# Kernel optimization log

Hardware: AMD Instinct MI355X
Metric: run time of the kernel (lower is better)

The kernel has to match this reference:

```python
import jax, jax.numpy as jnp
import numpy as np

SEQ_LEN = 2048   # configs.seq_len == h == KFSSM H
PRED_LEN = 720   # configs.pred_len == p
D_MODEL = 128    # configs.d_model == KFSSM N (complex state size N//2)
C_OUT = 64       # configs.c_out == channel dim of u
BATCH = 128


def setup_inputs() -> dict:
    key = jax.random.key(0)
    ks = jax.random.split(key, 12)
    H, n2, p = SEQ_LEN, D_MODEL // 2, PRED_LEN
    u = jax.random.normal(ks[0], (BATCH, SEQ_LEN, C_OUT), jnp.float32)
    x_mark_enc = jax.random.normal(ks[1], (BATCH, SEQ_LEN, 4), jnp.float32)
    x_dec = jax.random.normal(ks[2], (BATCH, PRED_LEN, C_OUT), jnp.float32)
    x_mark_dec = jax.random.normal(ks[3], (BATCH, PRED_LEN, 4), jnp.float32)
    # standard-normal noise; scaled by learned std inside reference (matches torch.normal(0, std))
    W_noise = jax.random.normal(ks[4], (BATCH, SEQ_LEN, C_OUT), jnp.float32)
    # Model params
    D = jax.random.normal(ks[5], (H,), jnp.float32)
    log_variance = jnp.log(1.0 + jax.random.uniform(ks[6], (1,), jnp.float32))
    # KFSSM params
    C_param = jax.random.normal(ks[7], (H, n2, 2), jnp.float32)  # view_as_real of complex C
    log_dt = (jax.random.uniform(ks[8], (H,), jnp.float32)
              * (np.log(0.1) - np.log(0.001)) + np.log(0.001))
    log_A_real = jnp.log(0.5 * jnp.ones((H, n2), jnp.float32))
    A_imag = np.pi * jnp.tile(jnp.arange(n2, dtype=jnp.float32)[None, :], (H, 1))
    # outporj: Linear(h -> 2p) then GLU(dim=2)
    proj_w = jax.random.normal(ks[9], (2 * p, H), jnp.float32) * 0.02
    proj_b = jnp.zeros((2 * p,), jnp.float32)
    return dict(u=u, x_mark_enc=x_mark_enc, x_dec=x_dec, x_mark_dec=x_mark_dec,
                W_noise=W_noise, D=D, log_variance=log_variance, C_param=C_param,
                log_dt=log_dt, log_A_real=log_A_real, A_imag=A_imag,
                proj_w=proj_w, proj_b=proj_b)


def _ssm_kernels(Nl, C_param, log_dt, log_A_real, A_imag):
    # KFSSM.forward(N=Nl): returns K, K2 of shape (H, Nl)
    dt = jnp.exp(log_dt)                              # (H,)
    C = C_param[..., 0] + 1j * C_param[..., 1]        # (H, n2)
    A = -jnp.exp(log_A_real) + 1j * A_imag            # (H, n2)
    ar = jnp.arange(Nl, dtype=log_dt.dtype)
    Bk = A[:, :1] * ar[None, :] * dt[:, None]         # (H, Nl) complex
    dtA = A * dt[:, None]                             # (H, n2)
    Kexp = jnp.exp(dtA[:, :, None] * ar[None, None, :])  # (H, n2, Nl)
    Cc = C * (jnp.exp(dtA) - 1.0) / A                 # (H, n2)
    K = 2.0 * jnp.einsum('hn,hnl->hl', Cc, Kexp).real # (H, Nl)
    K2 = 2.0 * (K * Bk).real                          # (H, Nl)
    return K, K2


def reference(u, x_mark_enc, x_dec, x_mark_dec, W_noise, D, log_variance,
              C_param, log_dt, log_A_real, A_imag, proj_w, proj_b):
    # instance normalization over time
    x_mean = jnp.mean(u, axis=1, keepdims=True)                  # (B,1,N)
    u0 = u - x_mean
    x_var = jnp.var(u0, axis=1, ddof=1, keepdims=True) + 1e-5    # unbiased, as torch.var
    un = u0 / jnp.sqrt(x_var)
    # Kalman process noise
    std = jnp.sqrt(jnp.exp(log_variance))                        # (1,)
    W = std * W_noise                                            # (B,L,N)
    l, Nch = un.shape[1], un.shape[2]
    nfft = 2 * l
    K, K2 = _ssm_kernels(Nch, C_param, log_dt, log_A_real, A_imag)  # (H=l, Nch)
    k_f = jnp.fft.rfft(K.T, n=nfft, axis=-1)                     # (Nch, l+1)
    k2_f = jnp.fft.rfft(K2.T, n=nfft, axis=-1)
    u_f = jnp.fft.rfft(jnp.transpose(un, (0, 2, 1)), n=nfft, axis=-1)   # (B,Nch,l+1)
    w_f = jnp.fft.rfft(jnp.transpose(W, (0, 2, 1)), n=nfft, axis=-1)
    y = (jnp.fft.irfft(u_f * k2_f, n=nfft, axis=-1)
         + jnp.fft.irfft(w_f * k_f, n=nfft, axis=-1))            # (B,Nch,2l)
    y = jnp.transpose(y, (0, 2, 1))[:, -l:, :] + un * D[:, None] # (B,l,Nch)
    # outporj: Linear(h->2p) over time axis, then GLU(dim=2); Dropout1d is identity at eval
    z = jnp.einsum('bnh,ph->bnp', jnp.transpose(y, (0, 2, 1)), proj_w) + proj_b  # (B,Nch,2p)
    a, b = jnp.split(z, 2, axis=2)
    y = jnp.transpose(a * jax.nn.sigmoid(b), (0, 2, 1))          # (B,p,Nch)
    y = y * jnp.sqrt(x_var) + x_mean
    return y[:, -PRED_LEN:, :]
```

## Files before the change

### kernel.cpp

```cpp
#include <hip/hip_runtime.h>
#include <math.h>

typedef unsigned short u16;
typedef unsigned int u32;
typedef __attribute__((ext_vector_type(8))) short short8;
typedef __attribute__((ext_vector_type(4))) float f32x4;

#define B_   128
#define L_   2048
#define C_   64
#define P_   720
#define P2_  1440
#define NPAD 1536
#define NFFT 4096
#define NROW (B_*C_)
#define TCHUNK 16

__device__ __forceinline__ u16 f2bf(float f) {
  union { float f; unsigned u; } x; x.f = f;
  unsigned r = x.u + 0x7fffu + ((x.u >> 16) & 1u);
  return (u16)(r >> 16);
}
__device__ __forceinline__ float bf2f_lo(u32 v) {
  union { unsigned u; float f; } x; x.u = v << 16; return x.f;
}
__device__ __forceinline__ float bf2f_hi(u32 v) {
  union { unsigned u; float f; } x; x.u = v & 0xffff0000u; return x.f;
}

__device__ __forceinline__ float2 cmul(float2 a, float2 b) {
  return make_float2(a.x * b.x - a.y * b.y, a.x * b.y + a.y * b.x);
}
__device__ __forceinline__ float2 cadd(float2 a, float2 b) { return make_float2(a.x + b.x, a.y + b.y); }
__device__ __forceinline__ float2 csub(float2 a, float2 b) { return make_float2(a.x - b.x, a.y - b.y); }

#define CSWAP(i, j) { float2 tt = a[i]; a[i] = a[j]; a[j] = tt; }

template<bool INV, bool HZ>
__device__ __forceinline__ void dft16(float2 a[16]) {
  const float S  = INV ? 1.f : -1.f;
  const float c1 = 0.9238795325112867f, s1 = 0.3826834323650898f, q2 = 0.7071067811865476f;
  const float2 W1 = make_float2( c1, S * s1), W2 = make_float2( q2, S * q2), W3 = make_float2( s1, S * c1);
  const float2 W5 = make_float2(-s1, S * c1), W6 = make_float2(-q2, S * q2), W7 = make_float2(-c1, S * s1);
  if (HZ) {
    a[8]  = a[0];
    a[9]  = cmul(a[1], W1);
    a[10] = cmul(a[2], W2);
    a[11] = cmul(a[3], W3);
    a[12] = make_float2(-S * a[4].y, S * a[4].x);
    a[13] = cmul(a[5], W5);
    a[14] = cmul(a[6], W6);
    a[15] = cmul(a[7], W7);
  } else {
    float2 t;
    t = csub(a[0], a[8]);  a[0] = cadd(a[0], a[8]);  a[8]  = t;
    t = csub(a[1], a[9]);  a[1] = cadd(a[1], a[9]);  a[9]  = cmul(t, W1);
    t = csub(a[2], a[10]); a[2] = cadd(a[2], a[10]); a[10] = cmul(t, W2);
    t = csub(a[3], a[11]); a[3] = cadd(a[3], a[11]); a[11] = cmul(t, W3);
    t = csub(a[4], a[12]); a[4] = cadd(a[4], a[12]); a[12] = make_float2(-S * t.y, S * t.x);
    t = csub(a[5], a[13]); a[5] = cadd(a[5], a[13]); a[13] = cmul(t, W5);
    t = csub(a[6], a[14]); a[6] = cadd(a[6], a[14]); a[14] = cmul(t, W6);
    t = csub(a[7], a[15]); a[7] = cadd(a[7], a[15]); a[15] = cmul(t, W7);
  }
#pragma unroll
  for (int h = 0; h < 16; h += 8) {
    float2 t;
    t = csub(a[h+0], a[h+4]); a[h+0] = cadd(a[h+0], a[h+4]); a[h+4] = t;
    t = csub(a[h+1], a[h+5]); a[h+1] = cadd(a[h+1], a[h+5]); a[h+5] = cmul(t, W2);
    t = csub(a[h+2], a[h+6]); a[h+2] = cadd(a[h+2], a[h+6]); a[h+6] = make_float2(-S * t.y, S * t.x);
    t = csub(a[h+3], a[h+7]); a[h+3] = cadd(a[h+3], a[h+7]); a[h+7] = cmul(t, W6);
  }
#pragma unroll
  for (int q = 0; q < 16; q += 4) {
    float2 t;
    t = csub(a[q+0], a[q+2]); a[q+0] = cadd(a[q+0], a[q+2]); a[q+2] = t;
    t = csub(a[q+1], a[q+3]); a[q+1] = cadd(a[q+1], a[q+3]); a[q+3] = make_float2(-S * t.y, S * t.x);
  }
#pragma unroll
  for (int p = 0; p < 16; p += 2) {
    float2 t = csub(a[p], a[p+1]); a[p] = cadd(a[p], a[p+1]); a[p+1] = t;
  }
  CSWAP(1, 8); CSWAP(2, 4); CSWAP(3, 12); CSWAP(5, 10); CSWAP(7, 14); CSWAP(11, 13);
}

__device__ __forceinline__ void twchain(float2 a[16], float2 w1) {
  float2 w2 = cmul(w1, w1);
  float2 w3 = cmul(w2, w1);
  float2 w4 = cmul(w2, w2);
  float2 w5 = cmul(w3, w2);
  float2 w6 = cmul(w3, w3);
  float2 w7 = cmul(w4, w3);
  float2 w8 = cmul(w4, w4);
  float2 w9 = cmul(w5, w4);
  float2 w10 = cmul(w5, w5);
  float2 w11 = cmul(w6, w5);
  float2 w12 = cmul(w6, w6);
  float2 w13 = cmul(w7, w6);
  float2 w14 = cmul(w7, w7);
  float2 w15 = cmul(w8, w7);
  a[1]  = cmul(a[1],  w1);  a[2]  = cmul(a[2],  w2);  a[3]  = cmul(a[3],  w3);
  a[4]  = cmul(a[4],  w4);  a[5]  = cmul(a[5],  w5);  a[6]  = cmul(a[6],  w6);
  a[7]  = cmul(a[7],  w7);  a[8]  = cmul(a[8],  w8);  a[9]  = cmul(a[9],  w9);
  a[10] = cmul(a[10], w10); a[11] = cmul(a[11], w11); a[12] = cmul(a[12], w12);
  a[13] = cmul(a[13], w13); a[14] = cmul(a[14], w14); a[15] = cmul(a[15], w15);
}

__device__ __forceinline__ void lds_wA(float2* X, const float2 r[16], int tid) {
  int base = (tid & 15) * 16 + ((tid >> 4) ^ ((tid & 7) << 1));
#pragma unroll
  for (int i = 0; i < 16; ++i) X[base + i * 256] = r[i];
}
__device__ __forceinline__ void lds_wB(float2* X, const float2 r[16], int tid) {
#pragma unroll
  for (int i = 0; i < 16; ++i)
    X[((tid & 0xF0) + i) * 16 + ((tid & 15) ^ ((i & 7) << 1))] = r[i];
}
__device__ __forceinline__ void lds_rd(const float2* X, float2 r[16], int tid) {
  const float4* X4 = (const float4*)X;
#pragma unroll
  for (int p = 0; p < 8; ++p) {
    float4 v = X4[tid * 8 + (p ^ (tid & 7))];
    r[2 * p]     = make_float2(v.x, v.y);
    r[2 * p + 1] = make_float2(v.z, v.w);
  }
}

__device__ __forceinline__ void fft_fwd_hz(float2 r[16], float2* X, int tid, const float2* twg) {
  dft16<false, true>(r);
  twchain(r, twg[tid]);
  lds_wA(X, r, tid);
  __syncthreads();
  lds_rd(X, r, tid);
  dft16<false, false>(r);
  twchain(r, twg[(tid & 15) << 4]);
  __syncthreads();
  lds_wB(X, r, tid);
  __syncthreads();
  lds_rd(X, r, tid);
  dft16<false, false>(r);
}

__device__ __forceinline__ void fft_inv(float2 r[16], float2* X, int tid, const float2* twg) {
  dft16<true, false>(r);
  __syncthreads();
  lds_wB(X, r, tid);
  __syncthreads();
  lds_rd(X, r, tid);
  float2 wb = twg[(tid & 15) << 4];
  twchain(r, make_float2(wb.x, -wb.y));
  dft16<true, false>(r);
  __syncthreads();
  lds_wA(X, r, tid);
  __syncthreads();
  lds_rd(X, r, tid);
  float2 wa = twg[tid];
  twchain(r, make_float2(wa.x, -wa.y));
  dft16<true, false>(r);
}

__global__ void k_twfill(float2* __restrict__ tw) {
  int k = threadIdx.x;
  double ang = -2.0 * 3.14159265358979323846 * (double)k / 4096.0;
  tw[k] = make_float2((float)cos(ang), (float)sin(ang));
}

__global__ void k_wconv(const float* __restrict__ pw, u16* __restrict__ wb) {
  size_t idx = (size_t)blockIdx.x * 256 + threadIdx.x;
  int n = (int)(idx >> 11);
  int k = (int)(idx & 2047);
  int q = n >> 1;
  float v = 0.f;
  if (q < P_) {
    int p = (n & 1) ? (P_ + q) : q;
    v = pw[(size_t)p * L_ + k];
  }
  wb[idx] = f2bf(v);
}

__global__ __launch_bounds__(256) void k_stats1(const float* __restrict__ u, float* __restrict__ ps,
                                                float* __restrict__ pq) {
  int blk = blockIdx.x;
  int b = blk >> 4, q = blk & 15;
  int tid = threadIdx.x;
  int c4 = tid & 15, g = tid >> 4;
  const float4* u4 = (const float4*)(u + ((size_t)b * L_ + q * 128) * C_);
  float4 s = make_float4(0.f, 0.f, 0.f, 0.f), sq = s;
#pragma unroll
  for (int i = 0; i < 8; ++i) {
    float4 v = u4[(size_t)(g + 16 * i) * 16 + c4];
    s.x += v.x; s.y += v.y; s.z += v.z; s.w += v.w;
    sq.x += v.x * v.x; sq.y += v.y * v.y; sq.z += v.z * v.z; sq.w += v.w * v.w;
  }
  __shared__ float4 sb[16][16], qb[16][16];
  sb[g][c4] = s; qb[g][c4] = sq;
  __syncthreads();
  if (g == 0) {
    float4 S = sb[0][c4], Q = qb[0][c4];
#pragma unroll
    for (int k = 1; k < 16; ++k) {
      float4 a = sb[k][c4], d = qb[k][c4];
      S.x += a.x; S.y += a.y; S.z += a.z; S.w += a.w;
      Q.x += d.x; Q.y += d.y; Q.z += d.z; Q.w += d.w;
    }
    ((float4*)ps)[blk * 16 + c4] = S;
    ((float4*)pq)[blk * 16 + c4] = Q;
  }
}

__global__ __launch_bounds__(256) void k_stats2(const float* __restrict__ ps, const float* __restrict__ pq,
                                                float4* __restrict__ mv) {
  int gid = blockIdx.x * 256 + threadIdx.x;
  int b = gid >> 6, c = gid & 63;
  float S = 0.f, Q = 0.f;
#pragma unroll
  for (int q = 0; q < 16; ++q) {
    S += ps[(size_t)(b * 16 + q) * 64 + c];
    Q += pq[(size_t)(b * 16 + q) * 64 + c];
  }
  float mean = S * (1.0f / 2048.0f);
  float var = (Q - S * S * (1.0f / 2048.0f)) * (1.0f / 2047.0f) + 1e-5f;
  float sv = sqrtf(var);
  mv[gid] = make_float4(mean, sv, 1.0f / sv, 0.0f);
}

__global__ __launch_bounds__(256) void k_ssmk(const float* __restrict__ Cp, const float* __restrict__ ldt,
                                              const float* __restrict__ lAr, const float* __restrict__ Aim,
                                              float2* __restrict__ kz) {
  int gid = blockIdx.x * 256 + threadIdx.x;
  int h = gid & 2047;
  int j = gid >> 11;
  float dt = expf(ldt[h]);
  float accx = 0.f;
  float Ar0 = 0.f;
  for (int n = 0; n < 64; ++n) {
    float Ar = -expf(lAr[h * 64 + n]);
    float Ai = Aim[h * 64 + n];
    if (n == 0) Ar0 = Ar;
    float dAr = Ar * dt, dAi = Ai * dt;
    float er = expf(dAr);
    float s1, c1; sincosf(dAi, &s1, &c1);
    float emr = er * c1 - 1.0f, emi = er * s1;
    float inv = 1.0f / (Ar * Ar + Ai * Ai);
    float qr = (emr * Ar + emi * Ai) * inv;
    float qi = (emi * Ar - emr * Ai) * inv;
    float cr = Cp[(size_t)(h * 64 + n) * 2];
    float ci = Cp[(size_t)(h * 64 + n) * 2 + 1];
    float ccr = cr * qr - ci * qi;
    float cci = cr * qi + ci * qr;
    float ej = expf(dAr * (float)j);
    float sj, cj; sincosf(dAi * (float)j, &sj, &cj);
    accx += ccr * (ej * cj) - cci * (ej * sj);
  }
  float K = 2.0f * accx;
  float K2 = 2.0f * K * (Ar0 * (float)j * dt);
  kz[(size_t)j * L_ + h] = make_float2(K2, -K);
}

__global__ __launch_bounds__(256) void k_packT(const float* __restrict__ u, const float* __restrict__ Wn,
                                               const float* __restrict__ lv, const float4* __restrict__ mv,
                                               u32* __restrict__ zu) {
  int b = blockIdx.x >> 5;
  int t0 = (blockIdx.x & 31) << 6;
  int tid = threadIdx.x;
  float stdn = sqrtf(__expf(lv[0]));
  __shared__ float2 tile[64][65];
  int c = tid & 63, r = tid >> 6;
  float4 m = mv[b * C_ + c];
#pragma unroll
  for (int i = 0; i < 16; ++i) {
    int t = t0 + i * 4 + r;
    size_t idx = ((size_t)b * L_ + t) * C_ + c;
    float uu = (u[idx] - m.x) * m.z;
    float ww = Wn[idx] * stdn;
    tile[i * 4 + r][c] = make_float2(uu, ww);
  }
  __syncthreads();
  int t = tid & 63, cb = tid >> 6;
#pragma unroll
  for (int i = 0; i < 16; ++i) {
    int c2 = i * 4 + cb;
    float2 v = tile[t][c2];
    zu[((size_t)(b * C_ + c2)) * L_ + t0 + t] = ((u32)f2bf(v.y) << 16) | (u32)f2bf(v.x);
  }
}

__global__ __launch_bounds__(256) void k_fftk(const float2* __restrict__ kz, const float2* __restrict__ twg,
                                              float2* __restrict__ G) {
  __shared__ float2 X[NFFT];
  int j = blockIdx.x, tid = threadIdx.x;
  float2 r[16];
#pragma unroll
  for (int n2 = 0; n2 < 8; ++n2) r[n2] = kz[(size_t)j * L_ + n2 * 256 + tid];
  fft_fwd_hz(r, X, tid, twg);
  const float sc = 1.0f / 4096.0f;
#pragma unroll
  for (int k0 = 0; k0 < 16; ++k0)
    G[(size_t)j * NFFT + k0 * 256 + tid] = make_float2(r[k0].x * sc, r[k0].y * sc);
}

__global__ __launch_bounds__(256) void k_fftmain(const u32* __restrict__ zu, const float2* __restrict__ twg,
                                                 const float2* __restrict__ G, const float* __restrict__ Dv,
                                                 u16* __restrict__ yT) {
  __shared__ float2 X[NFFT];
  int row = blockIdx.x;
  int j = row & 63;
  int tid = threadIdx.x;
  float2 r[16];
  float usav[8];
#pragma unroll
  for (int n2 = 0; n2 < 8; ++n2) {
    u32 v = zu[(size_t)row * L_ + n2 * 256 + tid];
    float uu = bf2f_lo(v), ww = bf2f_hi(v);
    r[n2] = make_float2(uu, ww);
    usav[n2] = uu;
  }
  fft_fwd_hz(r, X, tid, twg);
  const float2* Gj = G + (size_t)j * NFFT;
#pragma unroll
  for (int k0 = 0; k0 < 16; ++k0) r[k0] = cmul(r[k0], Gj[k0 * 256 + tid]);
  fft_inv(r, X, tid, twg);
#pragma unroll
  for (int n2 = 8; n2 < 16; ++n2) {
    int t = (n2 - 8) * 256 + tid;
    float yv = r[n2].x + usav[n2 - 8] * Dv[t];
    yT[(size_t)row * L_ + t] = f2bf(yv);
  }
}

__device__ __forceinline__ int lds_ix(int row, int slot) {
  return row * 32 + ((slot ^ ((row >> 1) & 3)) << 3);
}

__global__ __launch_bounds__(256) void k_gemm(const u16* __restrict__ A, const u16* __restrict__ B,
                                              const float* __restrict__ pb, const float4* __restrict__ mv,
                                              float* __restrict__ out) {
  __shared__ u16 As[128 * 32];
  __shared__ u16 Bs[128 * 32];
  __shared__ float ob[32 * 132];
  const int K = L_;
  int tid = threadIdx.x;
  int bid = blockIdx.x;
  int swz = (bid & 7) * 96 + (bid >> 3);
  int bm = swz % 64, bn = swz / 64;
  int wave = tid >> 6, lane = tid & 63;
  int wm = (wave >> 1) << 6, wn = (wave & 1) << 6;
  int lr = lane & 15, lk = lane >> 4;
  int trow = tid >> 2, tslot = tid & 3;
  const u16* Ag = A + (size_t)(bm * 128 + trow) * K + tslot * 8;
  const u16* Bg = B + (size_t)(bn * 128 + trow) * K + tslot * 8;
  f32x4 acc[4][4] = {};
  uint4 pa0 = *(const uint4*)(Ag);
  uint4 pa1 = *(const uint4*)(Ag + (size_t)64 * K);
  uint4 pb0 = *(const uint4*)(Bg);
  uint4 pb1 = *(const uint4*)(Bg + (size_t)64 * K);
  for (int kt = 0; kt < K; kt += 32) {
    __syncthreads();
    *(uint4*)&As[lds_ix(trow, tslot)] = pa0;
    *(uint4*)&As[lds_ix(trow + 64, tslot)] = pa1;
    *(uint4*)&Bs[lds_ix(trow, tslot)] = pb0;
    *(uint4*)&Bs[lds_ix(trow + 64, tslot)] = pb1;
    __syncthreads();
    if (kt + 32 < K) {
      pa0 = *(const uint4*)(Ag + kt + 32);
      pa1 = *(const uint4*)(Ag + (size_t)64 * K + kt + 32);
      pb0 = *(const uint4*)(Bg + kt + 32);
      pb1 = *(const uint4*)(Bg + (size_t)64 * K + kt + 32);
    }
    short8 af[4], bf[4];
#pragma unroll
    for (int i2 = 0; i2 < 4; ++i2) af[i2] = *(const short8*)&As[lds_ix(wm + i2 * 16 + lr, lk)];
#pragma unroll
    for (int j2 = 0; j2 < 4; ++j2) bf[j2] = *(const short8*)&Bs[lds_ix(wn + j2 * 16 + lr, lk)];
#pragma unroll
    for (int i2 = 0; i2 < 4; ++i2)
#pragma unroll
      for (int j2 = 0; j2 < 4; ++j2)
        acc[i2][j2] = __builtin_amdgcn_mfma_f32_16x16x32_bf16(af[i2], bf[j2], acc[i2][j2], 0, 0, 0);
  }
  int col_lo = wn + lr;
  for (int chunk = 0; chunk < 2; ++chunk) {
    __syncthreads();
#pragma unroll
    for (int j2c = 0; j2c < 2; ++j2c) {
      int j2 = chunk * 2 + j2c;
      int col = col_lo + j2 * 16;
      int nglob = bn * 128 + col;
      int q = nglob >> 1;
      float bias = 0.f;
      if (q < P_) bias = pb[(nglob & 1) ? (P_ + q) : q];
      int qloc = col >> 1;
      int s = (qloc & 15) | ((qloc >> 5) << 4);
#pragma unroll
      for (int i2 = 0; i2 < 4; ++i2) {
        int row = wm + i2 * 16 + lk * 4;
        float res[4];
#pragma unroll
        for (int rgi = 0; rgi < 4; ++rgi) {
          float val = acc[i2][j2][rgi] + bias;
          float other = __shfl_xor(val, 1);
          float4 m = mv[bm * 128 + row + rgi];
          res[rgi] = val * (1.0f / (1.0f + __expf(-other))) * m.y + m.x;
        }
        if (!(lane & 1)) {
          *(float4*)&ob[s * 132 + row] = make_float4(res[0], res[1], res[2], res[3]);
        }
      }
    }
    __syncthreads();
    int c = tid & 63, sl4 = tid >> 6;
    for (int rd = 0; rd < 16; ++rd) {
      int slice = rd * 4 + sl4;
      int s = slice >> 1, bb = slice & 1;
      int qloc = (s & 15) + chunk * 16 + ((s >> 4) << 5);
      int qglob = bn * 64 + qloc;
      if (qglob < P_) {
        int bg = bm * 2 + bb;
        out[((size_t)bg * P_ + qglob) * 64 + c] = ob[s * 132 + bb * 64 + c];
      }
    }
  }
}

extern "C" void kernel_launch(void* const* d_in, const int* in_sizes, int n_in,
                              void* d_out, int out_size, void* d_ws, size_t ws_size,
                              hipStream_t stream) {
  const float* u   = (const float*)d_in[0];
  const float* Wn  = (const float*)d_in[4];
  const float* Dv  = (const float*)d_in[5];
  const float* lv  = (const float*)d_in[6];
  const float* Cp  = (const float*)d_in[7];
  const float* ldt = (const float*)d_in[8];
  const float* lAr = (const float*)d_in[9];
  const float* Aim = (const float*)d_in[10];
  const float* pw  = (const float*)d_in[11];
  const float* pb  = (const float*)d_in[12];
  float* out = (float*)d_out;
  char* ws = (char*)d_ws;

  float2* tw = (float2*)(ws + 0);
  float4* mv = (float4*)(ws + (64 << 10));
  float2* G  = (float2*)(ws + (1 << 20));
  float2* kz = (float2*)(ws + (3 << 20));
  u16*    Wb = (u16*)   (ws + (4 << 20));
  float*  ps = (float*) (ws + (10 << 20));
  float*  pq = (float*) (ws + (10 << 20) + (512 << 10));
  u16*    yT = (u16*)   (ws + (16 << 20));
  u32*    zu = (u32*)   (ws + ((size_t)48 << 20));

  k_twfill<<<1, 256, 0, stream>>>(tw);
  k_wconv<<<(NPAD * L_) / 256, 256, 0, stream>>>(pw, Wb);
  k_stats1<<<B_ * TCHUNK, 256, 0, stream>>>(u, ps, pq);
  k_stats2<<<(B_ * C_) / 256, 256, 0, stream>>>(ps, pq, mv);
  k_ssmk<<<(C_ * L_) / 256, 256, 0, stream>>>(Cp, ldt, lAr, Aim, kz);
  k_packT<<<B_ * (L_ / 64), 256, 0, stream>>>(u, Wn, lv, mv, zu);
  k_fftk<<<C_, 256, 0, stream>>>(kz, tw, G);
  k_fftmain<<<NROW, 256, 0, stream>>>(zu, tw, G, Dv, yT);
  k_gemm<<<64 * (NPAD / 128), 256, 0, stream>>>(yT, Wb, pb, mv, out);
}
```

Measured before the change: 343.1 us.

## Merge independent prep kernels into two multi-role launches by block-index dispatch

Seven small setup kernels (twiddle fill, weight bf16 conversion, stats partials, stats finalize, SSM kernel generation, pack/transposition, kernel FFT) are combined into two launches. Blocks branch on blockIdx into roles, so independent work runs concurrently and launch gaps shrink. Each pack block recomputes the per-batch mean/var from the partial sums in LDS instead of waiting on a separate stats2 kernel. The full mv array is still written by extra blocks for the GEMM. The cost is redundant stats reduction work and a larger shared-memory footprint for every block in the merged kernel.

New measurement: 324.9 us. 5.3% less time.

```diff
diff --git a/kernel.cpp b/kernel.cpp
--- a/kernel.cpp
+++ b/kernel.cpp
@@ -15,6 +15,13 @@
 #define NFFT 4096
 #define NROW (B_*C_)
 #define TCHUNK 16
+
+#define PREP_SSMK   512
+#define PREP_STATS1 2048
+#define PREP_NB     (PREP_SSMK + PREP_STATS1 + 1 + (NPAD * L_) / 256)
+#define PF_PACK  4096
+#define PF_FFTK  64
+#define PF_NB    (PF_PACK + PF_FFTK + 32)
 
 __device__ __forceinline__ u16 f2bf(float f) {
   union { float f; unsigned u; } x; x.f = f;
@@ -158,144 +165,157 @@
   dft16<true, false>(r);
 }
 
-__global__ void k_twfill(float2* __restrict__ tw) {
-  int k = threadIdx.x;
-  double ang = -2.0 * 3.14159265358979323846 * (double)k / 4096.0;
-  tw[k] = make_float2((float)cos(ang), (float)sin(ang));
-}
-
-__global__ void k_wconv(const float* __restrict__ pw, u16* __restrict__ wb) {
-  size_t idx = (size_t)blockIdx.x * 256 + threadIdx.x;
-  int n = (int)(idx >> 11);
-  int k = (int)(idx & 2047);
-  int q = n >> 1;
-  float v = 0.f;
-  if (q < P_) {
-    int p = (n & 1) ? (P_ + q) : q;
-    v = pw[(size_t)p * L_ + k];
-  }
-  wb[idx] = f2bf(v);
-}
-
-__global__ __launch_bounds__(256) void k_stats1(const float* __restrict__ u, float* __restrict__ ps,
-                                                float* __restrict__ pq) {
-  int blk = blockIdx.x;
-  int b = blk >> 4, q = blk & 15;
-  int tid = threadIdx.x;
-  int c4 = tid & 15, g = tid >> 4;
-  const float4* u4 = (const float4*)(u + ((size_t)b * L_ + q * 128) * C_);
-  float4 s = make_float4(0.f, 0.f, 0.f, 0.f), sq = s;
-#pragma unroll
-  for (int i = 0; i < 8; ++i) {
-    float4 v = u4[(size_t)(g + 16 * i) * 16 + c4];
-    s.x += v.x; s.y += v.y; s.z += v.z; s.w += v.w;
-    sq.x += v.x * v.x; sq.y += v.y * v.y; sq.z += v.z * v.z; sq.w += v.w * v.w;
-  }
+__global__ __launch_bounds__(256) void k_prep(const float* __restrict__ pw, u16* __restrict__ wb,
+                                              const float* __restrict__ u, float* __restrict__ ps,
+                                              float* __restrict__ pq,
+                                              const float* __restrict__ Cp, const float* __restrict__ ldt,
+                                              const float* __restrict__ lAr, const float* __restrict__ Aim,
+                                              float2* __restrict__ kz, float2* __restrict__ tw) {
   __shared__ float4 sb[16][16], qb[16][16];
-  sb[g][c4] = s; qb[g][c4] = sq;
-  __syncthreads();
-  if (g == 0) {
-    float4 S = sb[0][c4], Q = qb[0][c4];
-#pragma unroll
-    for (int k = 1; k < 16; ++k) {
-      float4 a = sb[k][c4], d = qb[k][c4];
-      S.x += a.x; S.y += a.y; S.z += a.z; S.w += a.w;
-      Q.x += d.x; Q.y += d.y; Q.z += d.z; Q.w += d.w;
-    }
-    ((float4*)ps)[blk * 16 + c4] = S;
-    ((float4*)pq)[blk * 16 + c4] = Q;
-  }
-}
-
-__global__ __launch_bounds__(256) void k_stats2(const float* __restrict__ ps, const float* __restrict__ pq,
-                                                float4* __restrict__ mv) {
-  int gid = blockIdx.x * 256 + threadIdx.x;
-  int b = gid >> 6, c = gid & 63;
-  float S = 0.f, Q = 0.f;
-#pragma unroll
-  for (int q = 0; q < 16; ++q) {
-    S += ps[(size_t)(b * 16 + q) * 64 + c];
-    Q += pq[(size_t)(b * 16 + q) * 64 + c];
-  }
-  float mean = S * (1.0f / 2048.0f);
-  float var = (Q - S * S * (1.0f / 2048.0f)) * (1.0f / 2047.0f) + 1e-5f;
-  float sv = sqrtf(var);
-  mv[gid] = make_float4(mean, sv, 1.0f / sv, 0.0f);
-}
-
-__global__ __launch_bounds__(256) void k_ssmk(const float* __restrict__ Cp, const float* __restrict__ ldt,
-                                              const float* __restrict__ lAr, const float* __restrict__ Aim,
-                                              float2* __restrict__ kz) {
-  int gid = blockIdx.x * 256 + threadIdx.x;
-  int h = gid & 2047;
-  int j = gid >> 11;
-  float dt = expf(ldt[h]);
-  float accx = 0.f;
-  float Ar0 = 0.f;
-  for (int n = 0; n < 64; ++n) {
-    float Ar = -expf(lAr[h * 64 + n]);
-    float Ai = Aim[h * 64 + n];
-    if (n == 0) Ar0 = Ar;
-    float dAr = Ar * dt, dAi = Ai * dt;
-    float er = expf(dAr);
-    float s1, c1; sincosf(dAi, &s1, &c1);
-    float emr = er * c1 - 1.0f, emi = er * s1;
-    float inv = 1.0f / (Ar * Ar + Ai * Ai);
-    float qr = (emr * Ar + emi * Ai) * inv;
-    float qi = (emi * Ar - emr * Ai) * inv;
-    float cr = Cp[(size_t)(h * 64 + n) * 2];
-    float ci = Cp[(size_t)(h * 64 + n) * 2 + 1];
-    float ccr = cr * qr - ci * qi;
-    float cci = cr * qi + ci * qr;
-    float ej = expf(dAr * (float)j);
-    float sj, cj; sincosf(dAi * (float)j, &sj, &cj);
-    accx += ccr * (ej * cj) - cci * (ej * sj);
-  }
-  float K = 2.0f * accx;
-  float K2 = 2.0f * K * (Ar0 * (float)j * dt);
-  kz[(size_t)j * L_ + h] = make_float2(K2, -K);
-}
-
-__global__ __launch_bounds__(256) void k_packT(const float* __restrict__ u, const float* __restrict__ Wn,
-                                               const float* __restrict__ lv, const float4* __restrict__ mv,
-                                               u32* __restrict__ zu) {
-  int b = blockIdx.x >> 5;
-  int t0 = (blockIdx.x & 31) << 6;
-  int tid = threadIdx.x;
-  float stdn = sqrtf(__expf(lv[0]));
-  __shared__ float2 tile[64][65];
-  int c = tid & 63, r = tid >> 6;
-  float4 m = mv[b * C_ + c];
-#pragma unroll
-  for (int i = 0; i < 16; ++i) {
-    int t = t0 + i * 4 + r;
-    size_t idx = ((size_t)b * L_ + t) * C_ + c;
-    float uu = (u[idx] - m.x) * m.z;
-    float ww = Wn[idx] * stdn;
-    tile[i * 4 + r][c] = make_float2(uu, ww);
-  }
-  __syncthreads();
-  int t = tid & 63, cb = tid >> 6;
-#pragma unroll
-  for (int i = 0; i < 16; ++i) {
-    int c2 = i * 4 + cb;
-    float2 v = tile[t][c2];
-    zu[((size_t)(b * C_ + c2)) * L_ + t0 + t] = ((u32)f2bf(v.y) << 16) | (u32)f2bf(v.x);
-  }
-}
-
-__global__ __launch_bounds__(256) void k_fftk(const float2* __restrict__ kz, const float2* __restrict__ twg,
-                                              float2* __restrict__ G) {
-  __shared__ float2 X[NFFT];
-  int j = blockIdx.x, tid = threadIdx.x;
-  float2 r[16];
-#pragma unroll
-  for (int n2 = 0; n2 < 8; ++n2) r[n2] = kz[(size_t)j * L_ + n2 * 256 + tid];
-  fft_fwd_hz(r, X, tid, twg);
-  const float sc = 1.0f / 4096.0f;
-#pragma unroll
-  for (int k0 = 0; k0 < 16; ++k0)
-    G[(size_t)j * NFFT + k0 * 256 + tid] = make_float2(r[k0].x * sc, r[k0].y * sc);
+  int blk = blockIdx.x, tid = threadIdx.x;
+  if (blk < PREP_SSMK) {
+    int gid = blk * 256 + tid;
+    int h = gid & 2047;
+    int j = gid >> 11;
+    float dt = expf(ldt[h]);
+    float accx = 0.f;
+    float Ar0 = 0.f;
+    for (int n = 0; n < 64; ++n) {
+      float Ar = -expf(lAr[h * 64 + n]);
+      float Ai = Aim[h * 64 + n];
+      if (n == 0) Ar0 = Ar;
+      float dAr = Ar * dt, dAi = Ai * dt;
+      float er = expf(dAr);
+      float s1, c1; sincosf(dAi, &s1, &c1);
+      float emr = er * c1 - 1.0f, emi = er * s1;
+      float inv = 1.0f / (Ar * Ar + Ai * Ai);
+      float qr = (emr * Ar + emi * Ai) * inv;
+      float qi = (emi * Ar - emr * Ai) * inv;
+      float cr = Cp[(size_t)(h * 64 + n) * 2];
+      float ci = Cp[(size_t)(h * 64 + n) * 2 + 1];
+      float ccr = cr * qr - ci * qi;
+      float cci = cr * qi + ci * qr;
+      float ej = expf(dAr * (float)j);
+      float sj, cj; sincosf(dAi * (float)j, &sj, &cj);
+      accx += ccr * (ej * cj) - cci * (ej * sj);
+    }
+    float K = 2.0f * accx;
+    float K2 = 2.0f * K * (Ar0 * (float)j * dt);
+    kz[(size_t)j * L_ + h] = make_float2(K2, -K);
+  } else if (blk < PREP_SSMK + PREP_STATS1) {
+    int blk2 = blk - PREP_SSMK;
+    int b = blk2 >> 4, q = blk2 & 15;
+    int c4 = tid & 15, g = tid >> 4;
+    const float4* u4 = (const float4*)(u + ((size_t)b * L_ + q * 128) * C_);
+    float4 s = make_float4(0.f, 0.f, 0.f, 0.f), sq = s;
+#pragma unroll
+    for (int i = 0; i < 8; ++i) {
+      float4 v = u4[(size_t)(g + 16 * i) * 16 + c4];
+      s.x += v.x; s.y += v.y; s.z += v.z; s.w += v.w;
+      sq.x += v.x * v.x; sq.y += v.y * v.y; sq.z += v.z * v.z; sq.w += v.w * v.w;
+    }
+    sb[g][c4] = s; qb[g][c4] = sq;
+    __syncthreads();
+    if (g == 0) {
+      float4 S = sb[0][c4], Q = qb[0][c4];
+#pragma unroll
+      for (int k = 1; k < 16; ++k) {
+        float4 a = sb[k][c4], d = qb[k][c4];
+        S.x += a.x; S.y += a.y; S.z += a.z; S.w += a.w;
+        Q.x += d.x; Q.y += d.y; Q.z += d.z; Q.w += d.w;
+      }
+      ((float4*)ps)[blk2 * 16 + c4] = S;
+      ((float4*)pq)[blk2 * 16 + c4] = Q;
+    }
+  } else if (blk == PREP_SSMK + PREP_STATS1) {
+    int k = tid;
+    double ang = -2.0 * 3.14159265358979323846 * (double)k / 4096.0;
+    tw[k] = make_float2((float)cos(ang), (float)sin(ang));
+  } else {
+    size_t idx = (size_t)(blk - (PREP_SSMK + PREP_STATS1 + 1)) * 256 + tid;
+    int n = (int)(idx >> 11);
+    int k = (int)(idx & 2047);
+    int q = n >> 1;
+    float v = 0.f;
+    if (q < P_) {
+      int p = (n & 1) ? (P_ + q) : q;
+      v = pw[(size_t)p * L_ + k];
+    }
+    wb[idx] = f2bf(v);
+  }
+}
+
+__global__ __launch_bounds__(256) void k_packfftk(const float* __restrict__ u, const float* __restrict__ Wn,
+                                                  const float* __restrict__ lv,
+                                                  const float* __restrict__ ps, const float* __restrict__ pq,
+                                                  u32* __restrict__ zu,
+                                                  const float2* __restrict__ kz, const float2* __restrict__ twg,
+                                                  float2* __restrict__ G, float4* __restrict__ mv) {
+  __shared__ __align__(16) char smem[33280];
+  int blk = blockIdx.x, tid = threadIdx.x;
+  if (blk < PF_PACK) {
+    int b = blk >> 5;
+    int t0 = (blk & 31) << 6;
+    float4* mvs = (float4*)smem;
+    if (tid < 64) {
+      float S = 0.f, Q = 0.f;
+#pragma unroll
+      for (int q = 0; q < 16; ++q) {
+        S += ps[(size_t)(b * 16 + q) * 64 + tid];
+        Q += pq[(size_t)(b * 16 + q) * 64 + tid];
+      }
+      float mean = S * (1.0f / 2048.0f);
+      float var = (Q - S * S * (1.0f / 2048.0f)) * (1.0f / 2047.0f) + 1e-5f;
+      float sv = sqrtf(var);
+      mvs[tid] = make_float4(mean, sv, 1.0f / sv, 0.0f);
+    }
+    __syncthreads();
+    int c = tid & 63, r = tid >> 6;
+    float4 m = mvs[c];
+    float stdn = sqrtf(__expf(lv[0]));
+    __syncthreads();
+    float2 (*tile)[65] = (float2(*)[65])smem;
+#pragma unroll
+    for (int i = 0; i < 16; ++i) {
+      int t = t0 + i * 4 + r;
+      size_t idx = ((size_t)b * L_ + t) * C_ + c;
+      float uu = (u[idx] - m.x) * m.z;
+      float ww = Wn[idx] * stdn;
+      tile[i * 4 + r][c] = make_float2(uu, ww);
+    }
+    __syncthreads();
+    int t = tid & 63, cb = tid >> 6;
+#pragma unroll
+    for (int i = 0; i < 16; ++i) {
+      int c2 = i * 4 + cb;
+      float2 v = tile[t][c2];
+      zu[((size_t)(b * C_ + c2)) * L_ + t0 + t] = ((u32)f2bf(v.y) << 16) | (u32)f2bf(v.x);
+    }
+  } else if (blk < PF_PACK + PF_FFTK) {
+    float2* X = (float2*)smem;
+    int j = blk - PF_PACK;
+    float2 r[16];
+#pragma unroll
+    for (int n2 = 0; n2 < 8; ++n2) r[n2] = kz[(size_t)j * L_ + n2 * 256 + tid];
+    fft_fwd_hz(r, X, tid, twg);
+    const float sc = 1.0f / 4096.0f;
+#pragma unroll
+    for (int k0 = 0; k0 < 16; ++k0)
+      G[(size_t)j * NFFT + k0 * 256 + tid] = make_float2(r[k0].x * sc, r[k0].y * sc);
+  } else {
+    int gid = (blk - (PF_PACK + PF_FFTK)) * 256 + tid;
+    int b = gid >> 6, c = gid & 63;
+    float S = 0.f, Q = 0.f;
+#pragma unroll
+    for (int q = 0; q < 16; ++q) {
+      S += ps[(size_t)(b * 16 + q) * 64 + c];
+      Q += pq[(size_t)(b * 16 + q) * 64 + c];
+    }
+    float mean = S * (1.0f / 2048.0f);
+    float var = (Q - S * S * (1.0f / 2048.0f)) * (1.0f / 2047.0f) + 1e-5f;
+    float sv = sqrtf(var);
+    mv[gid] = make_float4(mean, sv, 1.0f / sv, 0.0f);
+  }
 }
 
 __global__ __launch_bounds__(256) void k_fftmain(const u32* __restrict__ zu, const float2* __restrict__ twg,
@@ -447,13 +467,8 @@
   u16*    yT = (u16*)   (ws + (16 << 20));
   u32*    zu = (u32*)   (ws + ((size_t)48 << 20));
 
-  k_twfill<<<1, 256, 0, stream>>>(tw);
-  k_wconv<<<(NPAD * L_) / 256, 256, 0, stream>>>(pw, Wb);
-  k_stats1<<<B_ * TCHUNK, 256, 0, stream>>>(u, ps, pq);
-  k_stats2<<<(B_ * C_) / 256, 256, 0, stream>>>(ps, pq, mv);
-  k_ssmk<<<(C_ * L_) / 256, 256, 0, stream>>>(Cp, ldt, lAr, Aim, kz);
-  k_packT<<<B_ * (L_ / 64), 256, 0, stream>>>(u, Wn, lv, mv, zu);
-  k_fftk<<<C_, 256, 0, stream>>>(kz, tw, G);
+  k_prep<<<PREP_NB, 256, 0, stream>>>(pw, Wb, u, ps, pq, Cp, ldt, lAr, Aim, kz, tw);
+  k_packfftk<<<PF_NB, 256, 0, stream>>>(u, Wn, lv, ps, pq, zu, kz, tw, G, mv);
   k_fftmain<<<NROW, 256, 0, stream>>>(zu, tw, G, Dv, yT);
   k_gemm<<<64 * (NPAD / 128), 256, 0, stream>>>(yT, Wb, pb, mv, out);
 }
```
